# Performance work log

Measured on AMD Instinct MI355X. Metric: run time of the kernel, lower is better.

## Reference

```python
import jax, jax.numpy as jnp
import numpy as np

N, D, N_CLASSES = 8192, 512, 128
POS_MARGIN = 1.0  # default path: sample_method=None, Dynamic_margin=None


def setup_inputs() -> dict:
    key = jax.random.key(0)
    k1, k2 = jax.random.split(key)
    x = jax.random.normal(k1, (N, D), dtype=jnp.float32)
    # metric-learning embeddings are L2-normalized so sim in [-1, 1]
    x = x / jnp.linalg.norm(x, axis=1, keepdims=True)
    targets = jax.random.randint(k2, (N,), 0, N_CLASSES, dtype=jnp.int64)
    return {"inputs": x, "targets": targets, "nonorm": 0}


def reference(inputs, targets, nonorm):
    n = inputs.shape[0]
    sim = jnp.matmul(inputs, inputs.T)                      # [n, n]
    same = targets[:, None] == targets[None, :]             # [n, n]
    pos_mask = same & (sim < POS_MARGIN)                    # drops self-sim == 1
    neg_mask = ~same

    # per-row masked log-sum-exp (sort in original is irrelevant to the sums)
    pos_sum = jnp.sum(jnp.where(pos_mask, jnp.exp(1.0 - sim), 0.0), axis=1)
    neg_sum = jnp.sum(jnp.where(neg_mask, jnp.exp(sim), 0.0), axis=1)
    pos_loss = jnp.log(pos_sum)
    neg_loss = jnp.log(neg_sum)

    has_neg = jnp.any(neg_mask, axis=1)                     # rows w/o negs are skipped
    loss = jnp.sum(jnp.where(has_neg, pos_loss + neg_loss, 0.0)) / n
    prec = jnp.mean(1.0 - has_neg.astype(jnp.float32))      # fraction of skipped rows

    # torch code reports means of the LAST row's pos/neg pairs
    last_pos = pos_mask[-1]
    last_neg = neg_mask[-1]
    mean_pos_sim = jnp.sum(jnp.where(last_pos, sim[-1], 0.0)) / jnp.sum(last_pos)
    mean_neg_sim = jnp.sum(jnp.where(last_neg, sim[-1], 0.0)) / jnp.sum(last_neg)
    return loss, prec, mean_pos_sim, mean_neg_sim
```

## Files before the change

kernel.cpp:

```cpp
#include <hip/hip_runtime.h>
#include <math.h>

#define N_ 8192
#define D_ 512
#define NC_ 128
#define T_ 64

typedef __attribute__((ext_vector_type(8))) short bf16x8;
typedef __attribute__((ext_vector_type(4))) float f32x4;
typedef __attribute__((ext_vector_type(4))) unsigned short us4;

static __device__ __forceinline__ unsigned short f2bf(float f) {
    union { float f; unsigned u; } c; c.f = f;
    unsigned u = c.u;
    u += 0x7fffu + ((u >> 16) & 1u);
    return (unsigned short)(u >> 16);
}

__global__ __launch_bounds__(256) void k_convert(const float* __restrict__ x,
                                                 unsigned short* __restrict__ xb) {
    int i = (blockIdx.x * 256 + threadIdx.x);
    float4 v = reinterpret_cast<const float4*>(x)[i];
    us4 o = { f2bf(v.x), f2bf(v.y), f2bf(v.z), f2bf(v.w) };
    reinterpret_cast<us4*>(xb)[i] = o;
}

__global__ __launch_bounds__(256, 2) void k_main(const unsigned short* __restrict__ xb,
                                                 const int* __restrict__ tg,
                                                 float* __restrict__ bufP,
                                                 float* __restrict__ bufN) {
    __shared__ alignas(16) unsigned short As[2][128 * 64];
    __shared__ alignas(16) unsigned short Bs[2][128 * 64];
    __shared__ int rowT[128];

    const int tid  = threadIdx.x;
    const int w    = tid >> 6;
    const int lane = tid & 63;
    const int q    = lane >> 4;
    const int l15  = lane & 15;
    const int wrow = w >> 1;
    const int wcol = w & 1;

    int rem = blockIdx.x;
    int it = 0;
    while (rem >= (T_ - it)) { rem -= (T_ - it); it++; }
    const int jt = it + rem;
    const int row0 = it * 128;
    const int col0 = jt * 128;

    auto STAGE = [&](int buf, int ks) {
        const int k0 = ks * 64;
        unsigned short* Ad = As[buf];
        unsigned short* Bd = Bs[buf];
#pragma unroll
        for (int itr = 0; itr < 4; ++itr) {
            int gs = (itr * 4 + w) * 64 + lane;
            int r  = gs >> 3;
            int s  = gs & 7;
            int g  = s ^ (r & 7);
            const unsigned short* ga = xb + (size_t)(row0 + r) * D_ + k0 + g * 8;
            const unsigned short* gb = xb + (size_t)(col0 + r) * D_ + k0 + g * 8;
            __builtin_amdgcn_global_load_lds(
                (const __attribute__((address_space(1))) void*)ga,
                (__attribute__((address_space(3))) void*)(Ad + (itr * 4 + w) * 512),
                16, 0, 0);
            __builtin_amdgcn_global_load_lds(
                (const __attribute__((address_space(1))) void*)gb,
                (__attribute__((address_space(3))) void*)(Bd + (itr * 4 + w) * 512),
                16, 0, 0);
        }
    };

    if (tid < 128) rowT[tid] = tg[row0 + tid];
    STAGE(0, 0);
    __syncthreads();

    int tR[4][4];
#pragma unroll
    for (int mi = 0; mi < 4; ++mi)
#pragma unroll
        for (int r = 0; r < 4; ++r)
            tR[mi][r] = rowT[wrow * 64 + mi * 16 + q * 4 + r];

    int tC[4];
#pragma unroll
    for (int ni = 0; ni < 4; ++ni)
        tC[ni] = tg[col0 + wcol * 64 + ni * 16 + l15];

    f32x4 acc[4][4];
#pragma unroll
    for (int mi = 0; mi < 4; ++mi)
#pragma unroll
        for (int ni = 0; ni < 4; ++ni)
            acc[mi][ni] = (f32x4){0.f, 0.f, 0.f, 0.f};

    auto COMPUTE = [&](int buf) {
        const unsigned short* A = As[buf];
        const unsigned short* B = Bs[buf];
#pragma unroll
        for (int kc = 0; kc < 2; ++kc) {
            bf16x8 aF[4], bF[4];
#pragma unroll
            for (int mi = 0; mi < 4; ++mi) {
                int rA = wrow * 64 + mi * 16 + l15;
                int g  = kc * 4 + q;
                int s  = g ^ (rA & 7);
                aF[mi] = *reinterpret_cast<const bf16x8*>(A + rA * 64 + s * 8);
            }
#pragma unroll
            for (int ni = 0; ni < 4; ++ni) {
                int rB = wcol * 64 + ni * 16 + l15;
                int g  = kc * 4 + q;
                int s  = g ^ (rB & 7);
                bF[ni] = *reinterpret_cast<const bf16x8*>(B + rB * 64 + s * 8);
            }
#pragma unroll
            for (int mi = 0; mi < 4; ++mi)
#pragma unroll
                for (int ni = 0; ni < 4; ++ni)
                    acc[mi][ni] = __builtin_amdgcn_mfma_f32_16x16x32_bf16(
                        aF[mi], bF[ni], acc[mi][ni], 0, 0, 0);
        }
    };

    int cur = 0;
#pragma unroll 1
    for (int ks = 0; ks < 7; ++ks) {
        STAGE(cur ^ 1, ks + 1);
        COMPUTE(cur);
        __syncthreads();
        cur ^= 1;
    }
    COMPUTE(cur);

    float ps[4][4], ns[4][4];
    float cps[4], cns[4];
#pragma unroll
    for (int mi = 0; mi < 4; ++mi)
#pragma unroll
        for (int r = 0; r < 4; ++r) { ps[mi][r] = 0.f; ns[mi][r] = 0.f; }
#pragma unroll
    for (int ni = 0; ni < 4; ++ni) { cps[ni] = 0.f; cns[ni] = 0.f; }

#pragma unroll
    for (int mi = 0; mi < 4; ++mi)
#pragma unroll
        for (int ni = 0; ni < 4; ++ni)
#pragma unroll
            for (int r = 0; r < 4; ++r) {
                float s = acc[mi][ni][r];
                bool same = (tR[mi][r] == tC[ni]);
                float e = __expf(same ? 1.0f - s : s);
                float pe = (same && (s < 1.0f)) ? e : 0.0f;
                float ne = same ? 0.0f : e;
                ps[mi][r] += pe; ns[mi][r] += ne;
                cps[ni]   += pe; cns[ni]   += ne;
            }

    __syncthreads();
    float* scr = (float*)As;

#pragma unroll
    for (int mi = 0; mi < 4; ++mi)
#pragma unroll
        for (int r = 0; r < 4; ++r) {
            float p = ps[mi][r];
            float n = ns[mi][r];
#pragma unroll
            for (int m = 1; m < 16; m <<= 1) {
                p += __shfl_xor(p, m, 64);
                n += __shfl_xor(n, m, 64);
            }
            if (l15 == 0) {
                int rloc = wrow * 64 + mi * 16 + q * 4 + r;
                scr[wcol * 128 + rloc]       = p;
                scr[256 + wcol * 128 + rloc] = n;
            }
        }

#pragma unroll
    for (int ni = 0; ni < 4; ++ni) {
        float p = cps[ni];
        float n = cns[ni];
        p += __shfl_xor(p, 16, 64); p += __shfl_xor(p, 32, 64);
        n += __shfl_xor(n, 16, 64); n += __shfl_xor(n, 32, 64);
        if (q == 0) {
            int cloc = wcol * 64 + ni * 16 + l15;
            scr[512 + wrow * 128 + cloc] = p;
            scr[768 + wrow * 128 + cloc] = n;
        }
    }
    __syncthreads();

    if (tid < 128) {
        int r = tid;
        size_t off = ((size_t)it * T_ + jt) * 128 + r;
        bufP[off] = scr[r]       + scr[128 + r];
        bufN[off] = scr[256 + r] + scr[384 + r];
    } else if (jt != it) {
        int c = tid - 128;
        size_t off = ((size_t)jt * T_ + it) * 128 + c;
        bufP[off] = scr[512 + c] + scr[640 + c];
        bufN[off] = scr[768 + c] + scr[896 + c];
    }
}

__global__ __launch_bounds__(256) void k_last(const float* __restrict__ x,
                                              double* __restrict__ sim_last) {
    int j    = (blockIdx.x * 256 + threadIdx.x) >> 6;
    int lane = threadIdx.x & 63;
    const float* xl = x + (size_t)(N_ - 1) * D_;
    const float* xj = x + (size_t)j * D_;
    double acc = 0.0;
#pragma unroll
    for (int it = 0; it < 8; ++it) {
        int k = it * 64 + lane;
        acc += (double)xl[k] * (double)xj[k];
    }
#pragma unroll
    for (int m = 32; m >= 1; m >>= 1) acc += __shfl_xor(acc, m, 64);
    if (lane == 0) sim_last[j] = acc;
}

__global__ __launch_bounds__(256) void k_reduce(const float* __restrict__ bufP,
                                                const float* __restrict__ bufN,
                                                float* __restrict__ psum,
                                                float* __restrict__ nsum) {
    int t    = blockIdx.x;
    int half = threadIdx.x >> 7;
    int r    = threadIdx.x & 127;
    const float* buf = half ? bufN : bufP;
    const float* base = buf + (size_t)t * T_ * 128 + r;
    float s = 0.f;
#pragma unroll
    for (int o = 0; o < T_; ++o) s += base[o * 128];
    if (half) nsum[t * 128 + r] = s;
    else      psum[t * 128 + r] = s;
}

__global__ __launch_bounds__(1024) void k_final(const float* __restrict__ psum,
                                                const float* __restrict__ nsum,
                                                const int* __restrict__ tg,
                                                const double* __restrict__ sim_last,
                                                float* __restrict__ out) {
    __shared__ int lh[NC_];
    __shared__ double sl[1024], sp[1024], sn[1024];
    __shared__ int    sk[1024], cp[1024], cn[1024];
    int tid = threadIdx.x;

    if (tid < NC_) lh[tid] = 0;
    __syncthreads();
    for (int i = tid; i < N_; i += 1024) atomicAdd(&lh[tg[i]], 1);
    __syncthreads();

    double part = 0.0;
    int skip = 0;
    for (int i = tid; i < N_; i += 1024) {
        if (lh[tg[i]] < N_) {
            part += (double)(logf(psum[i]) + logf(nsum[i]));
        } else {
            skip++;
        }
    }

    double pd = 0.0, nd = 0.0;
    int pc = 0, nc = 0;
    int tlast = tg[N_ - 1];
    for (int j = tid; j < N_; j += 1024) {
        double s = sim_last[j];
        if (tg[j] == tlast) {
            if (s < 1.0) { pd += s; pc++; }
        } else {
            nd += s; nc++;
        }
    }

    sl[tid] = part; sk[tid] = skip;
    sp[tid] = pd;   cp[tid] = pc;
    sn[tid] = nd;   cn[tid] = nc;
    __syncthreads();
    for (int s = 512; s >= 1; s >>= 1) {
        if (tid < s) {
            sl[tid] += sl[tid + s]; sk[tid] += sk[tid + s];
            sp[tid] += sp[tid + s]; cp[tid] += cp[tid + s];
            sn[tid] += sn[tid + s]; cn[tid] += cn[tid + s];
        }
        __syncthreads();
    }
    if (tid == 0) {
        out[0] = (float)(sl[0] / (double)N_);
        out[1] = (float)sk[0] / (float)N_;
        out[2] = (float)(sp[0] / (double)cp[0]);
        out[3] = (float)(sn[0] / (double)cn[0]);
    }
}

extern "C" void kernel_launch(void* const* d_in, const int* in_sizes, int n_in,
                              void* d_out, int out_size, void* d_ws, size_t ws_size,
                              hipStream_t stream) {
    const float* x  = (const float*)d_in[0];
    const int*   tg = (const int*)d_in[1];
    char* ws = (char*)d_ws;

    unsigned short* xb = (unsigned short*)ws;
    const size_t XB = (size_t)N_ * D_ * 2;
    float*  psum     = (float*)(ws + XB);
    float*  nsum     = (float*)(ws + XB + 32768);
    double* sim_last = (double*)(ws + XB + 65536);
    float*  bufP     = (float*)(ws + XB + 131072);
    float*  bufN     = (float*)(ws + XB + 131072 + 2097152);

    const int nblk_tri = T_ * (T_ + 1) / 2;

    hipLaunchKernelGGL(k_convert, dim3((N_ * D_) / (256 * 4)), dim3(256), 0, stream, x, xb);
    hipLaunchKernelGGL(k_main, dim3(nblk_tri), dim3(256), 0, stream, xb, tg, bufP, bufN);
    hipLaunchKernelGGL(k_last, dim3((N_ * 64) / 256), dim3(256), 0, stream, x, sim_last);
    hipLaunchKernelGGL(k_reduce, dim3(T_), dim3(256), 0, stream, bufP, bufN, psum, nsum);
    hipLaunchKernelGGL(k_final, dim3(1), dim3(1024), 0, stream,
                       psum, nsum, tg, sim_last, (float*)d_out);
}
```

Before: 156.4 us.

## Fuse prep kernels, shrink K-tile for occupancy, swizzle block order, parallelize final reduce

Merges bf16 conversion, last-row similarity and per-chunk class histograms into one pre-kernel, which removes a launch and moves histogram work out of the single-block final kernel. The main GEMM tile drops from BK 64 to 32 with a new swizzle and launch bounds of 4 blocks per CU. This halves LDS use per block so more blocks can be resident. Block IDs are remapped across the triangle to spread neighbouring tiles. The log/skip reduction moves into the 64-block reduce kernel, so the final kernel only sums 64 partials. The cost is twice as many k-steps with a barrier each, plus tighter register limits.

Result: faster. 152.8 us (-2.3%).

```diff
diff --git a/kernel.cpp b/kernel.cpp
--- a/kernel.cpp
+++ b/kernel.cpp
@@ -5,6 +5,8 @@
 #define D_ 512
 #define NC_ 128
 #define T_ 64
+#define BK_ 32
+#define KSTEPS 16
 
 typedef __attribute__((ext_vector_type(8))) short bf16x8;
 typedef __attribute__((ext_vector_type(4))) float f32x4;
@@ -17,20 +19,49 @@
     return (unsigned short)(u >> 16);
 }
 
-__global__ __launch_bounds__(256) void k_convert(const float* __restrict__ x,
-                                                 unsigned short* __restrict__ xb) {
-    int i = (blockIdx.x * 256 + threadIdx.x);
-    float4 v = reinterpret_cast<const float4*>(x)[i];
-    us4 o = { f2bf(v.x), f2bf(v.y), f2bf(v.z), f2bf(v.w) };
-    reinterpret_cast<us4*>(xb)[i] = o;
-}
-
-__global__ __launch_bounds__(256, 2) void k_main(const unsigned short* __restrict__ xb,
+__global__ __launch_bounds__(256) void k_pre(const float* __restrict__ x,
+                                             unsigned short* __restrict__ xb,
+                                             const int* __restrict__ tg,
+                                             double* __restrict__ sim_last,
+                                             int* __restrict__ hist32) {
+    const int bid = blockIdx.x;
+    const int tid = threadIdx.x;
+    if (bid < 4096) {
+        int i = bid * 256 + tid;
+        float4 v = reinterpret_cast<const float4*>(x)[i];
+        us4 o = { f2bf(v.x), f2bf(v.y), f2bf(v.z), f2bf(v.w) };
+        reinterpret_cast<us4*>(xb)[i] = o;
+    } else if (bid < 6144) {
+        int j    = (bid - 4096) * 4 + (tid >> 6);
+        int lane = tid & 63;
+        const float* xl = x + (size_t)(N_ - 1) * D_;
+        const float* xj = x + (size_t)j * D_;
+        double acc = 0.0;
+#pragma unroll
+        for (int it = 0; it < 8; ++it) {
+            int k = it * 64 + lane;
+            acc += (double)xl[k] * (double)xj[k];
+        }
+#pragma unroll
+        for (int m = 32; m >= 1; m >>= 1) acc += __shfl_xor(acc, m, 64);
+        if (lane == 0) sim_last[j] = acc;
+    } else {
+        __shared__ int lh[NC_];
+        int b = bid - 6144;
+        if (tid < NC_) lh[tid] = 0;
+        __syncthreads();
+        atomicAdd(&lh[tg[b * 256 + tid]], 1);
+        __syncthreads();
+        if (tid < NC_) hist32[b * NC_ + tid] = lh[tid];
+    }
+}
+
+__global__ __launch_bounds__(256, 4) void k_main(const unsigned short* __restrict__ xb,
                                                  const int* __restrict__ tg,
                                                  float* __restrict__ bufP,
                                                  float* __restrict__ bufN) {
-    __shared__ alignas(16) unsigned short As[2][128 * 64];
-    __shared__ alignas(16) unsigned short Bs[2][128 * 64];
+    __shared__ alignas(16) unsigned short As[2][128 * BK_];
+    __shared__ alignas(16) unsigned short Bs[2][128 * BK_];
     __shared__ int rowT[128];
 
     const int tid  = threadIdx.x;
@@ -41,7 +72,9 @@
     const int wrow = w >> 1;
     const int wcol = w & 1;
 
-    int rem = blockIdx.x;
+    const int bswz = (blockIdx.x & 7) * 260 + (blockIdx.x >> 3);
+
+    int rem = bswz;
     int it = 0;
     while (rem >= (T_ - it)) { rem -= (T_ - it); it++; }
     const int jt = it + rem;
@@ -49,24 +82,25 @@
     const int col0 = jt * 128;
 
     auto STAGE = [&](int buf, int ks) {
-        const int k0 = ks * 64;
+        const int k0 = ks * BK_;
         unsigned short* Ad = As[buf];
         unsigned short* Bd = Bs[buf];
 #pragma unroll
-        for (int itr = 0; itr < 4; ++itr) {
-            int gs = (itr * 4 + w) * 64 + lane;
-            int r  = gs >> 3;
-            int s  = gs & 7;
-            int g  = s ^ (r & 7);
+        for (int itr = 0; itr < 2; ++itr) {
+            int slot = itr * 4 + w;
+            int gs = slot * 64 + lane;
+            int r  = gs >> 2;
+            int sl = gs & 3;
+            int g  = sl ^ ((r >> 1) & 3);
             const unsigned short* ga = xb + (size_t)(row0 + r) * D_ + k0 + g * 8;
             const unsigned short* gb = xb + (size_t)(col0 + r) * D_ + k0 + g * 8;
             __builtin_amdgcn_global_load_lds(
                 (const __attribute__((address_space(1))) void*)ga,
-                (__attribute__((address_space(3))) void*)(Ad + (itr * 4 + w) * 512),
+                (__attribute__((address_space(3))) void*)(Ad + slot * 512),
                 16, 0, 0);
             __builtin_amdgcn_global_load_lds(
                 (const __attribute__((address_space(1))) void*)gb,
-                (__attribute__((address_space(3))) void*)(Bd + (itr * 4 + w) * 512),
+                (__attribute__((address_space(3))) void*)(Bd + slot * 512),
                 16, 0, 0);
         }
     };
@@ -97,35 +131,30 @@
     auto COMPUTE = [&](int buf) {
         const unsigned short* A = As[buf];
         const unsigned short* B = Bs[buf];
-#pragma unroll
-        for (int kc = 0; kc < 2; ++kc) {
-            bf16x8 aF[4], bF[4];
-#pragma unroll
-            for (int mi = 0; mi < 4; ++mi) {
-                int rA = wrow * 64 + mi * 16 + l15;
-                int g  = kc * 4 + q;
-                int s  = g ^ (rA & 7);
-                aF[mi] = *reinterpret_cast<const bf16x8*>(A + rA * 64 + s * 8);
-            }
-#pragma unroll
-            for (int ni = 0; ni < 4; ++ni) {
-                int rB = wcol * 64 + ni * 16 + l15;
-                int g  = kc * 4 + q;
-                int s  = g ^ (rB & 7);
-                bF[ni] = *reinterpret_cast<const bf16x8*>(B + rB * 64 + s * 8);
-            }
-#pragma unroll
-            for (int mi = 0; mi < 4; ++mi)
-#pragma unroll
-                for (int ni = 0; ni < 4; ++ni)
-                    acc[mi][ni] = __builtin_amdgcn_mfma_f32_16x16x32_bf16(
-                        aF[mi], bF[ni], acc[mi][ni], 0, 0, 0);
-        }
+        bf16x8 aF[4], bF[4];
+#pragma unroll
+        for (int mi = 0; mi < 4; ++mi) {
+            int rA = wrow * 64 + mi * 16 + l15;
+            int sl = q ^ ((rA >> 1) & 3);
+            aF[mi] = *reinterpret_cast<const bf16x8*>(A + rA * BK_ + sl * 8);
+        }
+#pragma unroll
+        for (int ni = 0; ni < 4; ++ni) {
+            int rB = wcol * 64 + ni * 16 + l15;
+            int sl = q ^ ((rB >> 1) & 3);
+            bF[ni] = *reinterpret_cast<const bf16x8*>(B + rB * BK_ + sl * 8);
+        }
+#pragma unroll
+        for (int mi = 0; mi < 4; ++mi)
+#pragma unroll
+            for (int ni = 0; ni < 4; ++ni)
+                acc[mi][ni] = __builtin_amdgcn_mfma_f32_16x16x32_bf16(
+                    aF[mi], bF[ni], acc[mi][ni], 0, 0, 0);
     };
 
     int cur = 0;
 #pragma unroll 1
-    for (int ks = 0; ks < 7; ++ks) {
+    for (int ks = 0; ks < KSTEPS - 1; ++ks) {
         STAGE(cur ^ 1, ks + 1);
         COMPUTE(cur);
         __syncthreads();
@@ -205,63 +234,58 @@
     }
 }
 
-__global__ __launch_bounds__(256) void k_last(const float* __restrict__ x,
-                                              double* __restrict__ sim_last) {
-    int j    = (blockIdx.x * 256 + threadIdx.x) >> 6;
-    int lane = threadIdx.x & 63;
-    const float* xl = x + (size_t)(N_ - 1) * D_;
-    const float* xj = x + (size_t)j * D_;
-    double acc = 0.0;
-#pragma unroll
-    for (int it = 0; it < 8; ++it) {
-        int k = it * 64 + lane;
-        acc += (double)xl[k] * (double)xj[k];
-    }
-#pragma unroll
-    for (int m = 32; m >= 1; m >>= 1) acc += __shfl_xor(acc, m, 64);
-    if (lane == 0) sim_last[j] = acc;
-}
-
 __global__ __launch_bounds__(256) void k_reduce(const float* __restrict__ bufP,
                                                 const float* __restrict__ bufN,
-                                                float* __restrict__ psum,
-                                                float* __restrict__ nsum) {
-    int t    = blockIdx.x;
-    int half = threadIdx.x >> 7;
-    int r    = threadIdx.x & 127;
+                                                const int* __restrict__ tg,
+                                                const int* __restrict__ hist32,
+                                                double* __restrict__ partd,
+                                                int* __restrict__ skipc) {
+    __shared__ float sv[256];
+    __shared__ int lh[NC_];
+    __shared__ double rd[128];
+    __shared__ int ri[128];
+    const int t   = blockIdx.x;
+    const int tid = threadIdx.x;
+    const int half = tid >> 7;
+    const int r    = tid & 127;
     const float* buf = half ? bufN : bufP;
     const float* base = buf + (size_t)t * T_ * 128 + r;
     float s = 0.f;
 #pragma unroll
     for (int o = 0; o < T_; ++o) s += base[o * 128];
-    if (half) nsum[t * 128 + r] = s;
-    else      psum[t * 128 + r] = s;
-}
-
-__global__ __launch_bounds__(1024) void k_final(const float* __restrict__ psum,
-                                                const float* __restrict__ nsum,
+    sv[tid] = s;
+    if (tid < NC_) {
+        int a = 0;
+#pragma unroll
+        for (int b = 0; b < 32; ++b) a += hist32[b * NC_ + tid];
+        lh[tid] = a;
+    }
+    __syncthreads();
+    if (tid < 128) {
+        int row = t * 128 + tid;
+        bool ok = lh[tg[row]] < N_;
+        rd[tid] = ok ? (double)(logf(sv[tid]) + logf(sv[128 + tid])) : 0.0;
+        ri[tid] = ok ? 0 : 1;
+    }
+    __syncthreads();
+    for (int st = 64; st >= 1; st >>= 1) {
+        if (tid < st) { rd[tid] += rd[tid + st]; ri[tid] += ri[tid + st]; }
+        __syncthreads();
+    }
+    if (tid == 0) { partd[t] = rd[0]; skipc[t] = ri[0]; }
+}
+
+__global__ __launch_bounds__(1024) void k_final(const double* __restrict__ partd,
+                                                const int* __restrict__ skipc,
                                                 const int* __restrict__ tg,
                                                 const double* __restrict__ sim_last,
                                                 float* __restrict__ out) {
-    __shared__ int lh[NC_];
     __shared__ double sl[1024], sp[1024], sn[1024];
     __shared__ int    sk[1024], cp[1024], cn[1024];
     int tid = threadIdx.x;
 
-    if (tid < NC_) lh[tid] = 0;
-    __syncthreads();
-    for (int i = tid; i < N_; i += 1024) atomicAdd(&lh[tg[i]], 1);
-    __syncthreads();
-
-    double part = 0.0;
-    int skip = 0;
-    for (int i = tid; i < N_; i += 1024) {
-        if (lh[tg[i]] < N_) {
-            part += (double)(logf(psum[i]) + logf(nsum[i]));
-        } else {
-            skip++;
-        }
-    }
+    double part = (tid < 64) ? partd[tid] : 0.0;
+    int    skip = (tid < 64) ? skipc[tid] : 0;
 
     double pd = 0.0, nd = 0.0;
     int pc = 0, nc = 0;
@@ -304,18 +328,20 @@
 
     unsigned short* xb = (unsigned short*)ws;
     const size_t XB = (size_t)N_ * D_ * 2;
-    float*  psum     = (float*)(ws + XB);
-    float*  nsum     = (float*)(ws + XB + 32768);
+    double* partd    = (double*)(ws + XB);
+    int*    skipc    = (int*)(ws + XB + 512);
+    int*    hist32   = (int*)(ws + XB + 1024);
     double* sim_last = (double*)(ws + XB + 65536);
     float*  bufP     = (float*)(ws + XB + 131072);
     float*  bufN     = (float*)(ws + XB + 131072 + 2097152);
 
     const int nblk_tri = T_ * (T_ + 1) / 2;
 
-    hipLaunchKernelGGL(k_convert, dim3((N_ * D_) / (256 * 4)), dim3(256), 0, stream, x, xb);
+    hipLaunchKernelGGL(k_pre, dim3(4096 + 2048 + 32), dim3(256), 0, stream,
+                       x, xb, tg, sim_last, hist32);
     hipLaunchKernelGGL(k_main, dim3(nblk_tri), dim3(256), 0, stream, xb, tg, bufP, bufN);
-    hipLaunchKernelGGL(k_last, dim3((N_ * 64) / 256), dim3(256), 0, stream, x, sim_last);
-    hipLaunchKernelGGL(k_reduce, dim3(T_), dim3(256), 0, stream, bufP, bufN, psum, nsum);
+    hipLaunchKernelGGL(k_reduce, dim3(T_), dim3(256), 0, stream,
+                       bufP, bufN, tg, hist32, partd, skipc);
     hipLaunchKernelGGL(k_final, dim3(1), dim3(1024), 0, stream,
-                       psum, nsum, tg, sim_last, (float*)d_out);
-}
+                       partd, skipc, tg, sim_last, (float*)d_out);
+}
```
